# Optimization experiments

Measured on AMD Instinct MI355X. Metric: run time of the kernel, lower is better.

## Reference

```python
import jax, jax.numpy as jnp
import numpy as np


def setup_inputs() -> dict:
    key = jax.random.key(0)
    k0, k1, k2, k3, k4 = jax.random.split(key, 5)
    B, d_inner, L, d_state = 64, 384, 197, 16
    x = jax.random.normal(k0, (B, d_inner, L), dtype=jnp.float32)
    # deltaA = exp(delta*A) lies in (0,1); uniform keeps the recurrence stable
    deltaA = jax.random.uniform(k1, (B, d_inner, L, d_state), dtype=jnp.float32)
    deltaB = jax.random.normal(k2, (B, d_inner, L, d_state), dtype=jnp.float32)
    C = jax.random.normal(k3, (B, d_state, L), dtype=jnp.float32)
    D = jax.random.normal(k4, (d_inner,), dtype=jnp.float32)
    return {"x": x, "deltaA": deltaA, "deltaB": deltaB, "C": C, "D": D}


def reference(x, deltaA, deltaB, C, D):
    """Selective scan: h_t = deltaB_t*x_t + deltaA_t*h_{t-1}; y_t = h_t @ C_t.
    x:(B,d,L) deltaA/deltaB:(B,d,L,n) C:(B,n,L) D:(d,)
    """
    deltaB_x = deltaB * x[..., None]              # (B,d,L,n)
    dA_t = jnp.moveaxis(deltaA, 2, 0)             # (L,B,d,n)
    dBx_t = jnp.moveaxis(deltaB_x, 2, 0)          # (L,B,d,n)
    C_t = jnp.moveaxis(C, 2, 0)                   # (L,B,n)

    def step(h, inputs):
        a, bx, c = inputs
        h = bx + a * h                            # (B,d,n)
        y = jnp.einsum("bdn,bn->bd", h, c)        # (B,d)
        return h, y

    h0 = jnp.zeros(dA_t.shape[1:], dtype=x.dtype)
    _, ys = jax.lax.scan(step, h0, (dA_t, dBx_t, C_t))  # ys: (L,B,d)
    y = jnp.moveaxis(ys, 0, 2)                    # (B,d,L)
    return y + x * D[:, None]
```

## Files before the change

kernel.cpp:

```cpp
#include <hip/hip_runtime.h>


#define B_   64
#define DIN  384
#define L_   197
#define N_   16
#define GROUPS_PER_BLOCK 16

__global__ __launch_bounds__(256)
void ssm_scan_kernel(const float* __restrict__ x,
                     const float* __restrict__ dA,
                     const float* __restrict__ dB,
                     const float* __restrict__ C,
                     const float* __restrict__ D,
                     float* __restrict__ y)
{
    __shared__ float Cs[N_ * L_];

    const int tid = threadIdx.x;
    const int b   = blockIdx.y;

    const float* Cg = C + (size_t)b * (N_ * L_);
    for (int i = tid; i < N_ * L_; i += 256) Cs[i] = Cg[i];
    __syncthreads();

    const int grp = tid >> 4;
    const int n   = tid & 15;
    const int d   = blockIdx.x * GROUPS_PER_BLOCK + grp;

    const size_t bd = (size_t)b * DIN + d;
    const float* pA = dA + bd * (size_t)(L_ * N_) + n;
    const float* pB = dB + bd * (size_t)(L_ * N_) + n;
    const float* px = x  + bd * L_;
    float*       py = y  + bd * L_;
    const float  Dd = D[d];
    const float* Cn = Cs + n * L_;

    float h = 0.0f;
    int t = 0;

    for (; t + 4 <= L_; t += 4) {
        const float a0 = pA[(t+0)*N_], a1 = pA[(t+1)*N_];
        const float a2 = pA[(t+2)*N_], a3 = pA[(t+3)*N_];
        const float g0 = pB[(t+0)*N_], g1 = pB[(t+1)*N_];
        const float g2 = pB[(t+2)*N_], g3 = pB[(t+3)*N_];
        const float x0 = px[t+0], x1 = px[t+1], x2 = px[t+2], x3 = px[t+3];
        const float c0 = Cn[t+0], c1 = Cn[t+1], c2 = Cn[t+2], c3 = Cn[t+3];

        h = fmaf(a0, h, g0 * x0);  float p0 = h * c0;
        h = fmaf(a1, h, g1 * x1);  float p1 = h * c1;
        h = fmaf(a2, h, g2 * x2);  float p2 = h * c2;
        h = fmaf(a3, h, g3 * x3);  float p3 = h * c3;

        #pragma unroll
        for (int m = 1; m < 16; m <<= 1) {
            p0 += __shfl_xor(p0, m);
            p1 += __shfl_xor(p1, m);
            p2 += __shfl_xor(p2, m);
            p3 += __shfl_xor(p3, m);
        }

        if (n == 0) {
            py[t+0] = fmaf(x0, Dd, p0);
            py[t+1] = fmaf(x1, Dd, p1);
            py[t+2] = fmaf(x2, Dd, p2);
            py[t+3] = fmaf(x3, Dd, p3);
        }
    }

    for (; t < L_; ++t) {
        const float a  = pA[t*N_];
        const float g  = pB[t*N_];
        const float xv = px[t];
        h = fmaf(a, h, g * xv);
        float p = h * Cn[t];
        #pragma unroll
        for (int m = 1; m < 16; m <<= 1) p += __shfl_xor(p, m);
        if (n == 0) py[t] = fmaf(xv, Dd, p);
    }
}

extern "C" void kernel_launch(void* const* d_in, const int* in_sizes, int n_in,
                              void* d_out, int out_size, void* d_ws, size_t ws_size,
                              hipStream_t stream) {
    const float* x  = (const float*)d_in[0];
    const float* dA = (const float*)d_in[1];
    const float* dB = (const float*)d_in[2];
    const float* C  = (const float*)d_in[3];
    const float* D  = (const float*)d_in[4];
    float* y = (float*)d_out;

    dim3 grid(DIN / GROUPS_PER_BLOCK, B_);
    dim3 block(256);
    ssm_scan_kernel<<<grid, block, 0, stream>>>(x, dA, dB, C, D, y);
}
```

Baseline: 162.8 us.

## Double-buffer deltaA/deltaB tiles into LDS via async global_load_lds with DPP reductions

Restructures the scan so each wave handles four channels and streams 16-timestep tiles of deltaA, deltaB and x into LDS with global_load_lds, double-buffered and synchronized by explicit vmcnt waits. The goal is to replace strided per-lane global loads with wide contiguous bursts that overlap the sequential recurrence. The 16-lane shuffle reduction becomes DPP adds, and outputs are collected in registers and written as one coalesced store per tile. C is transposed into LDS. Risks include lower occupancy from the larger LDS footprint and smaller blocks, fragile hand-tuned waitcnt counts, and an overlapping final tail tile.

```diff
diff --git a/kernel.cpp b/kernel.cpp
--- a/kernel.cpp
+++ b/kernel.cpp
@@ -5,79 +5,132 @@
 #define DIN  384
 #define L_   197
 #define N_   16
-#define GROUPS_PER_BLOCK 16
+#define BUFW 2176
+#define WAVEW (2*BUFW)
+#define CS_OFF (2*WAVEW)
+#define LDSW (CS_OFF + L_*N_)
 
-__global__ __launch_bounds__(256)
-void ssm_scan_kernel(const float* __restrict__ x,
-                     const float* __restrict__ dA,
-                     const float* __restrict__ dB,
-                     const float* __restrict__ C,
-                     const float* __restrict__ D,
-                     float* __restrict__ y)
+typedef unsigned int u32as1 __attribute__((address_space(1)));
+typedef unsigned int u32as3 __attribute__((address_space(3)));
+
+__device__ __forceinline__ void gll16(const float* g, float* l) {
+    __builtin_amdgcn_global_load_lds((const u32as1*)g, (u32as3*)l, 16, 0, 0);
+}
+__device__ __forceinline__ void gll4(const float* g, float* l) {
+    __builtin_amdgcn_global_load_lds((const u32as1*)g, (u32as3*)l, 4, 0, 0);
+}
+
+template<int CTRL>
+__device__ __forceinline__ float dppadd(float p) {
+    return p + __int_as_float(__builtin_amdgcn_update_dpp(
+        0, __float_as_int(p), CTRL, 0xF, 0xF, true));
+}
+__device__ __forceinline__ float sum16(float p) {
+    p = dppadd<0xB1>(p);
+    p = dppadd<0x4E>(p);
+    p = dppadd<0x141>(p);
+    p = dppadd<0x140>(p);
+    return p;
+}
+
+__global__ __launch_bounds__(128)
+void ssm_burst(const float* __restrict__ x, const float* __restrict__ dA,
+               const float* __restrict__ dB, const float* __restrict__ C,
+               const float* __restrict__ D, float* __restrict__ y)
 {
-    __shared__ float Cs[N_ * L_];
+    __shared__ __align__(16) float lds[LDSW];
 
     const int tid = threadIdx.x;
     const int b   = blockIdx.y;
+    const int d0  = blockIdx.x * 8;
 
     const float* Cg = C + (size_t)b * (N_ * L_);
-    for (int i = tid; i < N_ * L_; i += 256) Cs[i] = Cg[i];
+    for (int i = tid; i < N_ * L_; i += 128) {
+        const int n = i / L_;
+        const int t = i - n * L_;
+        lds[CS_OFF + t * N_ + n] = Cg[i];
+    }
     __syncthreads();
 
-    const int grp = tid >> 4;
-    const int n   = tid & 15;
-    const int d   = blockIdx.x * GROUPS_PER_BLOCK + grp;
+    const int wav  = tid >> 6;
+    const int lane = tid & 63;
+    const int g    = lane >> 4;
+    const int n    = lane & 15;
 
-    const size_t bd = (size_t)b * DIN + d;
-    const float* pA = dA + bd * (size_t)(L_ * N_) + n;
-    const float* pB = dB + bd * (size_t)(L_ * N_) + n;
-    const float* px = x  + bd * L_;
-    float*       py = y  + bd * L_;
-    const float  Dd = D[d];
-    const float* Cn = Cs + n * L_;
+    const int bd0 = b * DIN + d0 + wav * 4;
+    const float* Arow = dA + (size_t)bd0 * (L_ * N_);
+    const float* Brow = dB + (size_t)bd0 * (L_ * N_);
+    const float* Xrow = x  + (size_t)bd0 * L_;
+    float*       Yrow = y  + (size_t)(bd0 + g) * L_;
+    const float  Dd   = D[d0 + wav * 4 + g];
 
-    float h = 0.0f;
-    int t = 0;
+    float* wl = lds + wav * WAVEW;
+    const int lane4 = lane * 4;
 
-    for (; t + 4 <= L_; t += 4) {
-        const float a0 = pA[(t+0)*N_], a1 = pA[(t+1)*N_];
-        const float a2 = pA[(t+2)*N_], a3 = pA[(t+3)*N_];
-        const float g0 = pB[(t+0)*N_], g1 = pB[(t+1)*N_];
-        const float g2 = pB[(t+2)*N_], g3 = pB[(t+3)*N_];
-        const float x0 = px[t+0], x1 = px[t+1], x2 = px[t+2], x3 = px[t+3];
-        const float c0 = Cn[t+0], c1 = Cn[t+1], c2 = Cn[t+2], c3 = Cn[t+3];
+#define STAGE(buf, t0) do { \
+    float* _d = wl + (buf) * BUFW; \
+    gll16(Arow + 0*(L_*N_) + (t0)*16 + lane4, _d + 0*264); \
+    gll16(Arow + 1*(L_*N_) + (t0)*16 + lane4, _d + 1*264); \
+    gll16(Arow + 2*(L_*N_) + (t0)*16 + lane4, _d + 2*264); \
+    gll16(Arow + 3*(L_*N_) + (t0)*16 + lane4, _d + 3*264); \
+    gll16(Brow + 0*(L_*N_) + (t0)*16 + lane4, _d + 1056 + 0*264); \
+    gll16(Brow + 1*(L_*N_) + (t0)*16 + lane4, _d + 1056 + 1*264); \
+    gll16(Brow + 2*(L_*N_) + (t0)*16 + lane4, _d + 1056 + 2*264); \
+    gll16(Brow + 3*(L_*N_) + (t0)*16 + lane4, _d + 1056 + 3*264); \
+    gll4(Xrow + g * L_ + (t0) + n, _d + 2112); \
+} while (0)
 
-        h = fmaf(a0, h, g0 * x0);  float p0 = h * c0;
-        h = fmaf(a1, h, g1 * x1);  float p1 = h * c1;
-        h = fmaf(a2, h, g2 * x2);  float p2 = h * c2;
-        h = fmaf(a3, h, g3 * x3);  float p3 = h * c3;
+#define STEP(j, xv, tg0, J0) do { \
+    if ((j) >= (J0)) { \
+        const float _a = _ab[g*264 + (j)*16 + n]; \
+        const float _g = _ab[1056 + g*264 + (j)*16 + n]; \
+        h = fmaf(_a, h, _g * (xv)); \
+        float _p = h * lds[CS_OFF + ((tg0)+(j))*16 + n]; \
+        _p = sum16(_p); \
+        const float _yt = fmaf((xv), Dd, _p); \
+        _ys = (n == (j)) ? _yt : _ys; \
+    } \
+} while (0)
 
-        #pragma unroll
-        for (int m = 1; m < 16; m <<= 1) {
-            p0 += __shfl_xor(p0, m);
-            p1 += __shfl_xor(p1, m);
-            p2 += __shfl_xor(p2, m);
-            p3 += __shfl_xor(p3, m);
-        }
+#define TILEBODY(buf, tg0, J0) do { \
+    const float* _ab = wl + (buf) * BUFW; \
+    float _ys = 0.f; \
+    const float4 _x0 = *(const float4*)(_ab + 2112 + g*16 + 0); \
+    const float4 _x1 = *(const float4*)(_ab + 2112 + g*16 + 4); \
+    const float4 _x2 = *(const float4*)(_ab + 2112 + g*16 + 8); \
+    const float4 _x3 = *(const float4*)(_ab + 2112 + g*16 + 12); \
+    STEP( 0, _x0.x, tg0, J0); STEP( 1, _x0.y, tg0, J0); \
+    STEP( 2, _x0.z, tg0, J0); STEP( 3, _x0.w, tg0, J0); \
+    STEP( 4, _x1.x, tg0, J0); STEP( 5, _x1.y, tg0, J0); \
+    STEP( 6, _x1.z, tg0, J0); STEP( 7, _x1.w, tg0, J0); \
+    STEP( 8, _x2.x, tg0, J0); STEP( 9, _x2.y, tg0, J0); \
+    STEP(10, _x2.z, tg0, J0); STEP(11, _x2.w, tg0, J0); \
+    STEP(12, _x3.x, tg0, J0); STEP(13, _x3.y, tg0, J0); \
+    STEP(14, _x3.z, tg0, J0); STEP(15, _x3.w, tg0, J0); \
+    if ((J0) == 0) Yrow[(tg0) + n] = _ys; \
+    else if (n >= (J0)) Yrow[(tg0) + n] = _ys; \
+} while (0)
 
-        if (n == 0) {
-            py[t+0] = fmaf(x0, Dd, p0);
-            py[t+1] = fmaf(x1, Dd, p1);
-            py[t+2] = fmaf(x2, Dd, p2);
-            py[t+3] = fmaf(x3, Dd, p3);
-        }
+    float h = 0.f;
+
+    STAGE(0, 0);
+    STAGE(1, 16);
+    asm volatile("s_waitcnt vmcnt(9)" ::: "memory");
+    TILEBODY(0, 0, 0);
+
+#pragma unroll 1
+    for (int k = 1; k <= 11; ++k) {
+        const int tn = (k < 11) ? (k + 1) * 16 : 181;
+        STAGE((k + 1) & 1, tn);
+        asm volatile("s_waitcnt vmcnt(10)" ::: "memory");
+        TILEBODY(k & 1, k * 16, 0);
     }
+    asm volatile("s_waitcnt vmcnt(0)" ::: "memory");
+    TILEBODY(0, 181, 11);
 
-    for (; t < L_; ++t) {
-        const float a  = pA[t*N_];
-        const float g  = pB[t*N_];
-        const float xv = px[t];
-        h = fmaf(a, h, g * xv);
-        float p = h * Cn[t];
-        #pragma unroll
-        for (int m = 1; m < 16; m <<= 1) p += __shfl_xor(p, m);
-        if (n == 0) py[t] = fmaf(xv, Dd, p);
-    }
+#undef TILEBODY
+#undef STEP
+#undef STAGE
 }
 
 extern "C" void kernel_launch(void* const* d_in, const int* in_sizes, int n_in,
@@ -88,9 +141,9 @@
     const float* dB = (const float*)d_in[2];
     const float* C  = (const float*)d_in[3];
     const float* D  = (const float*)d_in[4];
-    float* y = (float*)d_out;
+    float* yo = (float*)d_out;
 
-    dim3 grid(DIN / GROUPS_PER_BLOCK, B_);
-    dim3 block(256);
-    ssm_scan_kernel<<<grid, block, 0, stream>>>(x, dA, dB, C, D, y);
+    dim3 grid(DIN / 8, B_);
+    dim3 block(128);
+    ssm_burst<<<grid, block, 0, stream>>>(x, dA, dB, C, D, yo);
 }
```

Result: faster. 142.5 us (-12.4%).
